# Performance work log

Hardware: AMD Instinct MI355X
Metric: run time of the kernel (lower is better)

The kernel has to match this reference:

```python
import jax, jax.numpy as jnp
import numpy as np

B, T, M, P = 256, 256, 256, 256  # batch, timesteps, encoder hidden m, decoder hidden p


def setup_inputs() -> dict:
    key = jax.random.key(0)
    ks = jax.random.split(key, 12)
    def n(k, shape, s=0.05):
        return jax.random.normal(k, shape, dtype=jnp.float32) * s
    return {
        "data": n(ks[0], (B, T - 1, 1), 1.0),          # decoder inputs y_1..y_{T-1}
        "encoder_h": n(ks[1], (B, T, M), 1.0),          # encoder hidden states
        "h0": jnp.zeros((B, P), jnp.float32),
        "s0": jnp.zeros((B, P), jnp.float32),
        # dense: Dense(1) on concat([x, context]) -> input dim 1+M
        "Wd": n(ks[2], (1 + M, 1)), "bd": jnp.zeros((1,), jnp.float32),
        # decoder LSTM (Keras gate order i,f,c,o): kernel (1,4P), recurrent (P,4P)
        "Wk": n(ks[3], (1, 4 * P)), "Wr": n(ks[4], (P, 4 * P)), "bl": jnp.zeros((4 * P,), jnp.float32),
        # temporal attention: W: 2P->M, U: M->M, v: M->1
        "Ww": n(ks[5], (2 * P, M)), "bw": jnp.zeros((M,), jnp.float32),
        "Wu": n(ks[6], (M, M)), "bu": jnp.zeros((M,), jnp.float32),
        "Wv": n(ks[7], (M, 1)), "bv": jnp.zeros((1,), jnp.float32),
        # output head: densevb: P+M -> 1, denseWb: 1 -> P
        "Wvb": n(ks[8], (P + M, 1)), "bvb": jnp.zeros((1,), jnp.float32),
        "Wwb": n(ks[9], (1, P)), "bwb": jnp.zeros((P,), jnp.float32),
    }


def reference(data, encoder_h, h0, s0, Wd, bd, Wk, Wr, bl, Ww, bw,
              Wu, bu, Wv, bv, Wvb, bvb, Wwb, bwb):
    # Hoist U(encoder_h) out of the time loop: it does not depend on t (same math).
    Ue = encoder_h @ Wu + bu                      # (B, T, M)
    xs = jnp.transpose(data, (1, 0, 2))           # (T-1, B, 1) for scan
    ctx0 = jnp.zeros((data.shape[0], Ue.shape[-1]), data.dtype)  # initial context (B, M)

    def step(carry, x_t):
        h, s, ctx = carry                          # (B,P), (B,P), (B,M)
        # y_tilde = Dense(1)(concat([x_t, context]))
        y = jnp.concatenate([x_t, ctx], axis=-1) @ Wd + bd        # (B, 1)
        # single-step Keras LSTM cell, gates i, f, c, o
        z = y @ Wk + h @ Wr + bl                   # (B, 4P)
        i, f, g, o = jnp.split(z, 4, axis=-1)
        s_new = jax.nn.sigmoid(f) * s + jax.nn.sigmoid(i) * jnp.tanh(g)
        h_new = jax.nn.sigmoid(o) * jnp.tanh(s_new)
        # temporal attention: l = v(tanh(W(repeat(concat[h,s])) + U(encoder_h)))
        dsc = jnp.concatenate([h_new, s_new], axis=-1) @ Ww + bw  # (B, M)
        l = jnp.tanh(dsc[:, None, :] + Ue) @ Wv + bv              # (B, T, 1)
        beta = jax.nn.softmax(l, axis=1)                          # softmax over time axis
        # context = beta^T @ encoder_h -> (B, M)
        ctx_new = jnp.sum(beta * encoder_h, axis=1)
        return (h_new, s_new, ctx_new), None

    (h, s, ctx), _ = jax.lax.scan(step, (h0, s0, ctx0), xs)
    cat = jnp.concatenate([h, ctx], axis=-1)[:, None, :]          # (B, 1, P+M)
    # denseWb(densevb(concatenated)): (P+M)->1 then 1->P, as in the source
    return (cat @ Wvb + bvb) @ Wwb + bwb                          # (B, 1, P)
```

## Files before the change

kernel.cpp:

```cpp
#include <hip/hip_runtime.h>
#include <hip/hip_bf16.h>

#define B 256
#define T 256
#define M 256
#define P 256
#define TSTEPS 255
#define NT 1024
#define RG 8

typedef unsigned int uint;
typedef _Float16 hf2 __attribute__((ext_vector_type(2)));

#define KEEP4(v) asm volatile("" : "+v"((v).x), "+v"((v).y), "+v"((v).z), "+v"((v).w))

__device__ __forceinline__ float fast_tanh(float x) {
    float e = exp2f(x * 2.885390082f);
    return 1.f - 2.f * __builtin_amdgcn_rcpf(e + 1.f);
}
__device__ __forceinline__ float fast_sigmoid(float x) {
    float e = exp2f(-x * 1.442695041f);
    return __builtin_amdgcn_rcpf(1.f + e);
}

#if defined(__has_builtin)
#if __has_builtin(__builtin_amdgcn_fdot2)
#define HAVE_FDOT2 1
#endif
#endif

__device__ __forceinline__ float dot2(uint a, uint b, float c) {
#ifdef HAVE_FDOT2
    return __builtin_amdgcn_fdot2(__builtin_bit_cast(hf2, a),
                                  __builtin_bit_cast(hf2, b), c, false);
#else
    hf2 x = __builtin_bit_cast(hf2, a), y = __builtin_bit_cast(hf2, b);
    return c + (float)x.x * (float)y.x + (float)x.y * (float)y.y;
#endif
}

__device__ __forceinline__ uint pk16(float a, float b) {
    return __builtin_bit_cast(uint, __builtin_amdgcn_cvt_pkrtz(a, b));
}

__device__ __forceinline__ uint pkmulsq(uint a, uint b) {
    uint p;
    asm("v_pk_mul_f16 %0, %1, %2\n\t"
        "v_pk_mul_f16 %0, %0, %0" : "=v"(p) : "v"(a), "v"(b));
    return p;
}

__device__ __forceinline__ float rcp1p(float x) {
    return __builtin_amdgcn_rcpf(x + 1.f);
}

__device__ __forceinline__ void fsig(int* f, int lane) {
    __threadfence_block();
    if (lane == 0) atomicAdd(f, 1);
}
__device__ __forceinline__ void fwait(int* f, int tgt) {
    while (*(volatile int*)f < tgt) __builtin_amdgcn_s_sleep(1);
    __threadfence_block();
}

__global__ __launch_bounds__(256) void ue_gemm(
    const float* __restrict__ enc, const float* __restrict__ Wu,
    const float* __restrict__ bu, _Float16* __restrict__ Ue16)
{
    __shared__ float At[32][256];
    const int r0 = blockIdx.x * 32;
    const int tid = threadIdx.x;

    #pragma unroll 4
    for (int i = 0; i < 32; ++i)
        At[i][tid] = enc[(size_t)(r0 + i) * 256 + tid];
    __syncthreads();

    float acc[32];
    #pragma unroll
    for (int r = 0; r < 32; ++r) acc[r] = 0.f;

    for (int k = 0; k < 256; k += 4) {
        float w0 = Wu[(size_t)(k + 0) * 256 + tid];
        float w1 = Wu[(size_t)(k + 1) * 256 + tid];
        float w2 = Wu[(size_t)(k + 2) * 256 + tid];
        float w3 = Wu[(size_t)(k + 3) * 256 + tid];
        #pragma unroll
        for (int r = 0; r < 32; ++r) {
            float4 a4 = *(const float4*)&At[r][k];
            acc[r] += a4.x * w0 + a4.y * w1 + a4.z * w2 + a4.w * w3;
        }
    }
    float bub = bu[tid];
    #pragma unroll 4
    for (int r = 0; r < 32; ++r)
        Ue16[(size_t)(r0 + r) * 256 + tid] =
            (_Float16)exp2f(1.442695041f * (acc[r] + bub));
}

__global__ __launch_bounds__(256) void wr_cvt(
    const float* __restrict__ Wr, uint4* __restrict__ Wsz)
{
    int i = blockIdx.x * 256 + threadIdx.x;
    int kc = i >> 10, c = i & 1023;
    const float* s = Wr + (size_t)kc * 8 * 1024 + c;
    uint4 o;
    o.x = pk16(s[0 * 1024], s[1 * 1024]);
    o.y = pk16(s[2 * 1024], s[3 * 1024]);
    o.z = pk16(s[4 * 1024], s[5 * 1024]);
    o.w = pk16(s[6 * 1024], s[7 * 1024]);
    Wsz[i] = o;
}

__global__ __launch_bounds__(256) void ww_cvt(
    const float* __restrict__ Ww, uint4* __restrict__ Wwsz)
{
    int i = blockIdx.x * 256 + threadIdx.x;
    int kk = i >> 8, m = i & 255;
    const float* s = Ww + (size_t)kk * 8 * 256 + m;
    uint4 o;
    o.x = pk16(s[0 * 256], s[1 * 256]);
    o.y = pk16(s[2 * 256], s[3 * 256]);
    o.z = pk16(s[4 * 256], s[5 * 256]);
    o.w = pk16(s[6 * 256], s[7 * 256]);
    Wwsz[i] = o;
}

__global__ __launch_bounds__(NT, 4) void decoder_scan(
    const float* __restrict__ data,
    const float* __restrict__ h0,  const float* __restrict__ s0,
    const float* __restrict__ Wd,  const float* __restrict__ bd,
    const float* __restrict__ Wk,  const float* __restrict__ bl,
    const float* __restrict__ bw,
    const float* __restrict__ Wv,  const float* __restrict__ bv,
    const float* __restrict__ Wvb, const float* __restrict__ bvb,
    const float* __restrict__ Wwb, const float* __restrict__ bwb,
    const float* __restrict__ enc,
    const _Float16* __restrict__ Ue16g,
    const uint4* __restrict__ Wsz, const uint4* __restrict__ Wwsz,
    float* __restrict__ out)
{
    const int b    = blockIdx.x;
    const int tid  = threadIdx.x;
    const int lane = tid & 63;
    const int wave = tid >> 6;

    __shared__ __align__(16) uint4 ww_lds[2 * 16 * 256];
    __shared__ float h_lds[P], s_lds[P];
    __shared__ __align__(16) uint hs2[128 + 4 + 128];
    __shared__ float z_lds[4 * 257];
    __shared__ __align__(16) uint  edup[2][132];
    __shared__ __align__(16) float wv2dup[2][264];
    __shared__ float el_lds[T];
    __shared__ float g_lds[T];
    __shared__ float ctx_lds[M];
    __shared__ __align__(16) float sred[8], yred[8];
    __shared__ float ya[4];
    __shared__ float data_lds[TSTEPS + 1];
    __shared__ int pf, zf, ef, df;

    uint* h2_lds = hs2;
    uint* s2_lds = hs2 + 132;

    {
        #pragma unroll
        for (int k = 0; k < 8; ++k) {
            int l = tid + k * NT;
            int i = l >> 9, r = l & 511, dmm = r >> 1, dk = r & 1;
            ww_lds[l] = Wwsz[((dk * 32 + i) << 8) + dmm];
        }
    }
    if (tid == 0) { pf = 0; zf = 0; ef = 0; df = 0; }
    if (tid < 256) {
        float hv = h0[b * 256 + tid], sv = s0[b * 256 + tid];
        h_lds[tid] = hv; s_lds[tid] = sv; ctx_lds[tid] = 0.f;
        float w2 = 2.f * Wv[tid];
        wv2dup[0][tid] = w2; wv2dup[1][tid] = w2;
        float hv1 = __shfl_down(hv, 1, 64);
        float sv1 = __shfl_down(sv, 1, 64);
        if (!(tid & 1)) {
            h2_lds[tid >> 1] = pk16(hv, hv1);
            s2_lds[tid >> 1] = pk16(sv, sv1);
        }
    }
    if (tid < 8) { sred[tid] = 1.f; yred[tid] = 0.f; }
    if (tid < TSTEPS) data_lds[tid] = data[b * TSTEPS + tid];

    const float Wd0 = Wd[0], bd0 = bd[0];
    const float* encB = enc + (size_t)b * T * M;

    {
        float w0 = Wd[1 + lane * 4], w1 = Wd[2 + lane * 4];
        float w2 = Wd[3 + lane * 4], w3 = Wd[4 + lane * 4];
        for (int i = 0; i < 16; ++i) {
            int tp = wave * 16 + i;
            float4 e4 = *(const float4*)&encB[(size_t)tp * 256 + lane * 4];
            float p = e4.x * w0 + e4.y * w1 + e4.z * w2 + e4.w * w3;
            #pragma unroll
            for (int mm = 32; mm >= 1; mm >>= 1) p += __shfl_xor(p, mm, 64);
            if (lane == 0) g_lds[tp] = p;
        }
    }
    __syncthreads();

    const uint4* h2u4 = (const uint4*)h2_lds;
    const uint4* s2u4 = (const uint4*)s2_lds;

    {
        const uint4* wc = Wsz + tid;
        float acc = 0.f;
        #pragma unroll 4
        for (int kc = 0; kc < 32; ++kc) {
            uint4 w = wc[kc << 10];
            uint4 h = h2u4[kc];
            acc = dot2(w.x, h.x, acc); acc = dot2(w.y, h.y, acc);
            acc = dot2(w.z, h.z, acc); acc = dot2(w.w, h.w, acc);
        }
        z_lds[(tid >> 8) * 257 + (tid & 255)] = acc;
    }
    __syncthreads();

    if (wave < 8) {
        const int gate = tid & 3, uu0 = tid >> 2, uu1 = uu0 + 128;
        const int cz0 = gate * 257 + uu0, cz1 = gate * 257 + uu1;
        const float wk0 = Wk[gate * 256 + uu0], bl0 = bl[gate * 256 + uu0];
        const float wk1 = Wk[gate * 256 + uu1], bl1 = bl[gate * 256 + uu1];
        const int zr = tid >> 8, zc = tid & 255;
        const uint4* wcA = Wsz + tid;
        const uint4* wcB = Wsz + tid + 512;
        uint4 rA[RG], rB[RG];
        #pragma unroll
        for (int kc = 0; kc < RG; ++kc) {
            rA[kc] = wcA[kc << 10]; rB[kc] = wcB[kc << 10];
            KEEP4(rA[kc]); KEEP4(rB[kc]);
        }

        for (int t = 0; t < TSTEPS; ++t) {
            uint4 pA0 = wcA[(RG + 0) << 10], pB0 = wcB[(RG + 0) << 10];
            uint4 pA1 = wcA[(RG + 1) << 10], pB1 = wcB[(RG + 1) << 10];

            fwait(&zf, 8 * t);
            fwait(&ef, 8 * t);
            {
                float4 sa = *(const float4*)&sred[0], sb = *(const float4*)&sred[4];
                float4 yaa = *(const float4*)&yred[0], yab = *(const float4*)&yred[4];
                float S = sa.x + sa.y + sa.z + sa.w + sb.x + sb.y + sb.z + sb.w;
                float Y = yaa.x + yaa.y + yaa.z + yaa.w + yab.x + yab.y + yab.z + yab.w;
                float ys = Y * __builtin_amdgcn_rcpf(S) + data_lds[t] * Wd0 + bd0;
                float zc0 = z_lds[cz0] + ys * wk0 + bl0;
                float zc1 = z_lds[cz1] + ys * wk1 + bl1;
                float nl0 = (gate == 2) ? fast_tanh(zc0) : fast_sigmoid(zc0);
                float nl1 = (gate == 2) ? fast_tanh(zc1) : fast_sigmoid(zc1);
                float a1 = __shfl_xor(nl0, 1, 64);
                float a2 = __shfl_xor(nl0, 2, 64);
                float a3 = __shfl_xor(nl0, 3, 64);
                float b1 = __shfl_xor(nl1, 1, 64);
                float b2 = __shfl_xor(nl1, 2, 64);
                float b3 = __shfl_xor(nl1, 3, 64);
                float hn0 = 0.f, sv0 = 0.f, hn1 = 0.f, sv1 = 0.f;
                if (gate == 0) {
                    sv0 = a1 * s_lds[uu0] + nl0 * a2;
                    hn0 = a3 * fast_tanh(sv0);
                    sv1 = b1 * s_lds[uu1] + nl1 * b2;
                    hn1 = b3 * fast_tanh(sv1);
                    s_lds[uu0] = sv0; h_lds[uu0] = hn0;
                    s_lds[uu1] = sv1; h_lds[uu1] = hn1;
                }
                float hd0 = __shfl_down(hn0, 4, 64), sd0 = __shfl_down(sv0, 4, 64);
                float hd1 = __shfl_down(hn1, 4, 64), sd1 = __shfl_down(sv1, 4, 64);
                if ((tid & 7) == 0) {
                    h2_lds[uu0 >> 1] = pk16(hn0, hd0); s2_lds[uu0 >> 1] = pk16(sv0, sd0);
                    h2_lds[uu1 >> 1] = pk16(hn1, hd1); s2_lds[uu1 >> 1] = pk16(sv1, sd1);
                }
            }
            fsig(&pf, lane);
            fwait(&pf, 8 * (t + 1));

            float a0 = 0.f, a1 = 0.f;
            #pragma unroll
            for (int kc = 0; kc < RG; ++kc) {
                uint4 h = h2u4[kc];
                a0 = dot2(rA[kc].x, h.x, a0); a0 = dot2(rA[kc].y, h.y, a0);
                a0 = dot2(rA[kc].z, h.z, a0); a0 = dot2(rA[kc].w, h.w, a0);
                a1 = dot2(rB[kc].x, h.x, a1); a1 = dot2(rB[kc].y, h.y, a1);
                a1 = dot2(rB[kc].z, h.z, a1); a1 = dot2(rB[kc].w, h.w, a1);
            }
            {
                uint4 h = h2u4[RG];
                a0 = dot2(pA0.x, h.x, a0); a0 = dot2(pA0.y, h.y, a0);
                a0 = dot2(pA0.z, h.z, a0); a0 = dot2(pA0.w, h.w, a0);
                a1 = dot2(pB0.x, h.x, a1); a1 = dot2(pB0.y, h.y, a1);
                a1 = dot2(pB0.z, h.z, a1); a1 = dot2(pB0.w, h.w, a1);
            }
            {
                uint4 h = h2u4[RG + 1];
                a0 = dot2(pA1.x, h.x, a0); a0 = dot2(pA1.y, h.y, a0);
                a0 = dot2(pA1.z, h.z, a0); a0 = dot2(pA1.w, h.w, a0);
                a1 = dot2(pB1.x, h.x, a1); a1 = dot2(pB1.y, h.y, a1);
                a1 = dot2(pB1.z, h.z, a1); a1 = dot2(pB1.w, h.w, a1);
            }
            #pragma unroll 4
            for (int kc = RG + 2; kc < 32; ++kc) {
                uint4 wA = wcA[kc << 10], wB = wcB[kc << 10];
                uint4 h = h2u4[kc];
                a0 = dot2(wA.x, h.x, a0); a0 = dot2(wA.y, h.y, a0);
                a0 = dot2(wA.z, h.z, a0); a0 = dot2(wA.w, h.w, a0);
                a1 = dot2(wB.x, h.x, a1); a1 = dot2(wB.y, h.y, a1);
                a1 = dot2(wB.z, h.z, a1); a1 = dot2(wB.w, h.w, a1);
            }
            z_lds[zr * 257 + zc] = a0;
            z_lds[(2 + zr) * 257 + zc] = a1;
            fsig(&zf, lane);
        }
    } else {
        const int aw  = wave - 8;
        const int aid = tid - 512;
        const int dm  = aid >> 1;
        const int dkh = aid & 1;
        const float bwm = bw[dm];
        const uint4* wwp  = Wwsz + (dkh << 13) + dm;
        const uint4* wwl  = ww_lds + aid;
        const uint4*  edT = (const uint4*)(&edup[dkh][0]) + (dkh << 4);
        const float4* wvT = (const float4*)(&wv2dup[dkh][0]) + (dkh << 5);
        const uint4* cat4 = dkh ? s2u4 : h2u4;

        uint4 eu[16];
        {
            const uint4* eusrc = (const uint4*)(Ue16g + (size_t)b * T * M) + (aid << 4);
            #pragma unroll
            for (int i = 0; i < 16; ++i) { eu[i] = eusrc[i]; KEEP4(eu[i]); }
        }

        for (int t = 0; t < TSTEPS; ++t) {
            uint4 e0 = wwp[16 << 8], e1 = wwp[17 << 8];
            uint4 e2 = wwp[18 << 8], e3 = wwp[19 << 8];
            fwait(&pf, 8 * (t + 1));
            float a = 0.f;
            #pragma unroll 4
            for (int i = 0; i < 16; ++i) {
                uint4 w = wwl[i << 9];
                uint4 c = cat4[i];
                a = dot2(w.x, c.x, a); a = dot2(w.y, c.y, a);
                a = dot2(w.z, c.z, a); a = dot2(w.w, c.w, a);
            }
            {
                uint4 c = cat4[16];
                a = dot2(e0.x, c.x, a); a = dot2(e0.y, c.y, a);
                a = dot2(e0.z, c.z, a); a = dot2(e0.w, c.w, a);
                c = cat4[17];
                a = dot2(e1.x, c.x, a); a = dot2(e1.y, c.y, a);
                a = dot2(e1.z, c.z, a); a = dot2(e1.w, c.w, a);
                c = cat4[18];
                a = dot2(e2.x, c.x, a); a = dot2(e2.y, c.y, a);
                a = dot2(e2.z, c.z, a); a = dot2(e2.w, c.w, a);
                c = cat4[19];
                a = dot2(e3.x, c.x, a); a = dot2(e3.y, c.y, a);
                a = dot2(e3.z, c.z, a); a = dot2(e3.w, c.w, a);
            }
            #pragma unroll 4
            for (int i = 20; i < 32; ++i) {
                uint4 w = wwp[i << 8];
                uint4 c = cat4[i];
                a = dot2(w.x, c.x, a); a = dot2(w.y, c.y, a);
                a = dot2(w.z, c.z, a); a = dot2(w.w, c.w, a);
            }
            a += __shfl_xor(a, 1, 64);
            float ed = exp2f(1.442695041f * (a + bwm));
            float ed2 = __shfl_xor(ed, 2, 64);
            if ((aid & 3) == 0) {
                uint u = pk16(ed, ed2);
                edup[0][dm >> 1] = u;
                edup[1][dm >> 1] = u;
            }
            fsig(&df, lane);
            fwait(&df, 8 * (t + 1));

            __builtin_amdgcn_s_setprio(1);
            float pl = 0.f;
            #pragma unroll
            for (int jj = 0; jj < 16; ++jj) {
                uint4 u = eu[jj];
                uint4 d = edT[jj];
                float4 wA = wvT[jj * 2], wB = wvT[jj * 2 + 1];
                uint q0 = pkmulsq(u.x, d.x);
                uint q1 = pkmulsq(u.y, d.y);
                uint q2 = pkmulsq(u.z, d.z);
                uint q3 = pkmulsq(u.w, d.w);
                hf2 g0 = __builtin_bit_cast(hf2, q0);
                hf2 g1 = __builtin_bit_cast(hf2, q1);
                hf2 g2 = __builtin_bit_cast(hf2, q2);
                hf2 g3 = __builtin_bit_cast(hf2, q3);
                pl = fmaf(wA.x, rcp1p((float)g0.x), pl);
                pl = fmaf(wA.y, rcp1p((float)g0.y), pl);
                pl = fmaf(wA.z, rcp1p((float)g1.x), pl);
                pl = fmaf(wA.w, rcp1p((float)g1.y), pl);
                pl = fmaf(wB.x, rcp1p((float)g2.x), pl);
                pl = fmaf(wB.y, rcp1p((float)g2.y), pl);
                pl = fmaf(wB.z, rcp1p((float)g3.x), pl);
                pl = fmaf(wB.w, rcp1p((float)g3.y), pl);
            }
            pl += __shfl_xor(pl, 1, 64);
            float ev = exp2f(-1.442695041f * pl);
            if (!dkh) el_lds[dm] = ev;
            float yg = ev * g_lds[dm];
            #pragma unroll
            for (int mm = 2; mm <= 32; mm <<= 1) {
                ev += __shfl_xor(ev, mm, 64);
                yg += __shfl_xor(yg, mm, 64);
            }
            if (lane == 0) { sred[aw] = ev; yred[aw] = yg; }
            __builtin_amdgcn_s_setprio(0);
            fsig(&ef, lane);
        }
    }

    __syncthreads();

    {
        float S;
        {
            float4 sa = *(const float4*)&sred[0], sb = *(const float4*)&sred[4];
            S = sa.x + sa.y + sa.z + sa.w + sb.x + sb.y + sb.z + sb.w;
        }
        float a0 = 0.f, a1 = 0.f, a2 = 0.f, a3 = 0.f;
        for (int i = 0; i < 16; ++i) {
            int tp = wave * 16 + i;
            float w = el_lds[tp];
            float4 e4 = *(const float4*)&encB[(size_t)tp * 256 + lane * 4];
            a0 += w * e4.x; a1 += w * e4.y; a2 += w * e4.z; a3 += w * e4.w;
        }
        atomicAdd(&ctx_lds[lane * 4 + 0], a0);
        atomicAdd(&ctx_lds[lane * 4 + 1], a1);
        atomicAdd(&ctx_lds[lane * 4 + 2], a2);
        atomicAdd(&ctx_lds[lane * 4 + 3], a3);
        __syncthreads();

        float qp = 0.f;
        if (tid < 256) {
            float ctx = ctx_lds[tid] * __builtin_amdgcn_rcpf(S);
            qp = h_lds[tid] * Wvb[tid] + ctx * Wvb[256 + tid];
        }
        if (wave < 4) {
            #pragma unroll
            for (int mm = 32; mm >= 1; mm >>= 1) qp += __shfl_xor(qp, mm, 64);
            if (lane == 0) ya[wave] = qp;
        }
        __syncthreads();
        if (tid < 256) {
            float qv = ya[0] + ya[1] + ya[2] + ya[3] + bvb[0];
            out[b * 256 + tid] = qv * Wwb[tid] + bwb[tid];
        }
    }
}

extern "C" void kernel_launch(void* const* d_in, const int* in_sizes, int n_in,
                              void* d_out, int out_size, void* d_ws, size_t ws_size,
                              hipStream_t stream) {
    const float* data = (const float*)d_in[0];
    const float* enc  = (const float*)d_in[1];
    const float* h0   = (const float*)d_in[2];
    const float* s0   = (const float*)d_in[3];
    const float* Wd   = (const float*)d_in[4];
    const float* bd   = (const float*)d_in[5];
    const float* Wk   = (const float*)d_in[6];
    const float* Wr   = (const float*)d_in[7];
    const float* bl   = (const float*)d_in[8];
    const float* Ww   = (const float*)d_in[9];
    const float* bw   = (const float*)d_in[10];
    const float* Wu   = (const float*)d_in[11];
    const float* bu   = (const float*)d_in[12];
    const float* Wv   = (const float*)d_in[13];
    const float* bv   = (const float*)d_in[14];
    const float* Wvb  = (const float*)d_in[15];
    const float* bvb  = (const float*)d_in[16];
    const float* Wwb  = (const float*)d_in[17];
    const float* bwb  = (const float*)d_in[18];

    _Float16* Ue16 = (_Float16*)d_ws;
    uint4* Wsz  = (uint4*)((char*)d_ws + (32ull << 20));
    uint4* Wwsz = (uint4*)((char*)d_ws + (32ull << 20) + (512ull << 10));
    float* out = (float*)d_out;

    hipLaunchKernelGGL(ue_gemm, dim3((B * T) / 32), dim3(256), 0, stream,
                       enc, Wu, bu, Ue16);
    hipLaunchKernelGGL(wr_cvt, dim3(128), dim3(256), 0, stream, Wr, Wsz);
    hipLaunchKernelGGL(ww_cvt, dim3(64), dim3(256), 0, stream, Ww, Wwsz);
    hipLaunchKernelGGL(decoder_scan, dim3(B), dim3(NT), 0, stream,
                       data, h0, s0, Wd, bd, Wk, bl, bw,
                       Wv, bv, Wvb, bvb, Wwb, bwb,
                       enc, Ue16, Wsz, Wwsz, out);
}
```

Before: 2.395 ms.

## Pin resident weights in AGPRs and software-pipeline streamed recurrent weight loads

Register-resident Wr slices and half of the cached Ue16 values are now held in accumulator registers (AGPRs) rather than VGPRs, and the resident chunk count drops from 8 to 4. The remaining recurrent-weight chunks are streamed in groups of four, with the next group's global loads issued before the current group's dot products, so load latency overlaps compute. The inline-asm packed multiply is replaced by plain half-vector multiplies the compiler can schedule. The cost is more global weight traffic per step and possible AGPR-to-VGPR copies on every use.

```diff
diff --git a/kernel.cpp b/kernel.cpp
--- a/kernel.cpp
+++ b/kernel.cpp
@@ -7,12 +7,13 @@
 #define P 256
 #define TSTEPS 255
 #define NT 1024
-#define RG 8
+#define RG 4
 
 typedef unsigned int uint;
 typedef _Float16 hf2 __attribute__((ext_vector_type(2)));
 
-#define KEEP4(v) asm volatile("" : "+v"((v).x), "+v"((v).y), "+v"((v).z), "+v"((v).w))
+#define KEEP4A(v) asm volatile("" : "+a"((v).x), "+a"((v).y), "+a"((v).z), "+a"((v).w))
+#define KEEP4V(v) asm volatile("" : "+v"((v).x), "+v"((v).y), "+v"((v).z), "+v"((v).w))
 
 __device__ __forceinline__ float fast_tanh(float x) {
     float e = exp2f(x * 2.885390082f);
@@ -41,13 +42,6 @@
 
 __device__ __forceinline__ uint pk16(float a, float b) {
     return __builtin_bit_cast(uint, __builtin_amdgcn_cvt_pkrtz(a, b));
-}
-
-__device__ __forceinline__ uint pkmulsq(uint a, uint b) {
-    uint p;
-    asm("v_pk_mul_f16 %0, %1, %2\n\t"
-        "v_pk_mul_f16 %0, %0, %0" : "=v"(p) : "v"(a), "v"(b));
-    return p;
 }
 
 __device__ __forceinline__ float rcp1p(float x) {
@@ -232,12 +226,15 @@
         #pragma unroll
         for (int kc = 0; kc < RG; ++kc) {
             rA[kc] = wcA[kc << 10]; rB[kc] = wcB[kc << 10];
-            KEEP4(rA[kc]); KEEP4(rB[kc]);
+            KEEP4A(rA[kc]); KEEP4A(rB[kc]);
         }
 
         for (int t = 0; t < TSTEPS; ++t) {
-            uint4 pA0 = wcA[(RG + 0) << 10], pB0 = wcB[(RG + 0) << 10];
-            uint4 pA1 = wcA[(RG + 1) << 10], pB1 = wcB[(RG + 1) << 10];
+            uint4 sA[4], sB[4];
+            #pragma unroll
+            for (int i = 0; i < 4; ++i) {
+                sA[i] = wcA[(RG + i) << 10]; sB[i] = wcB[(RG + i) << 10];
+            }
 
             fwait(&zf, 8 * t);
             fwait(&ef, 8 * t);
@@ -285,28 +282,26 @@
                 a1 = dot2(rB[kc].x, h.x, a1); a1 = dot2(rB[kc].y, h.y, a1);
                 a1 = dot2(rB[kc].z, h.z, a1); a1 = dot2(rB[kc].w, h.w, a1);
             }
-            {
-                uint4 h = h2u4[RG];
-                a0 = dot2(pA0.x, h.x, a0); a0 = dot2(pA0.y, h.y, a0);
-                a0 = dot2(pA0.z, h.z, a0); a0 = dot2(pA0.w, h.w, a0);
-                a1 = dot2(pB0.x, h.x, a1); a1 = dot2(pB0.y, h.y, a1);
-                a1 = dot2(pB0.z, h.z, a1); a1 = dot2(pB0.w, h.w, a1);
-            }
-            {
-                uint4 h = h2u4[RG + 1];
-                a0 = dot2(pA1.x, h.x, a0); a0 = dot2(pA1.y, h.y, a0);
-                a0 = dot2(pA1.z, h.z, a0); a0 = dot2(pA1.w, h.w, a0);
-                a1 = dot2(pB1.x, h.x, a1); a1 = dot2(pB1.y, h.y, a1);
-                a1 = dot2(pB1.z, h.z, a1); a1 = dot2(pB1.w, h.w, a1);
-            }
-            #pragma unroll 4
-            for (int kc = RG + 2; kc < 32; ++kc) {
-                uint4 wA = wcA[kc << 10], wB = wcB[kc << 10];
-                uint4 h = h2u4[kc];
-                a0 = dot2(wA.x, h.x, a0); a0 = dot2(wA.y, h.y, a0);
-                a0 = dot2(wA.z, h.z, a0); a0 = dot2(wA.w, h.w, a0);
-                a1 = dot2(wB.x, h.x, a1); a1 = dot2(wB.y, h.y, a1);
-                a1 = dot2(wB.z, h.z, a1); a1 = dot2(wB.w, h.w, a1);
+            #pragma unroll
+            for (int g = 0; g < 7; ++g) {
+                uint4 nA[4], nB[4];
+                if (g < 6) {
+                    #pragma unroll
+                    for (int i = 0; i < 4; ++i) {
+                        nA[i] = wcA[(RG + 4 * (g + 1) + i) << 10];
+                        nB[i] = wcB[(RG + 4 * (g + 1) + i) << 10];
+                    }
+                }
+                #pragma unroll
+                for (int i = 0; i < 4; ++i) {
+                    uint4 h = h2u4[RG + 4 * g + i];
+                    a0 = dot2(sA[i].x, h.x, a0); a0 = dot2(sA[i].y, h.y, a0);
+                    a0 = dot2(sA[i].z, h.z, a0); a0 = dot2(sA[i].w, h.w, a0);
+                    a1 = dot2(sB[i].x, h.x, a1); a1 = dot2(sB[i].y, h.y, a1);
+                    a1 = dot2(sB[i].z, h.z, a1); a1 = dot2(sB[i].w, h.w, a1);
+                }
+                #pragma unroll
+                for (int i = 0; i < 4; ++i) { sA[i] = nA[i]; sB[i] = nB[i]; }
             }
             z_lds[zr * 257 + zc] = a0;
             z_lds[(2 + zr) * 257 + zc] = a1;
@@ -328,7 +323,9 @@
         {
             const uint4* eusrc = (const uint4*)(Ue16g + (size_t)b * T * M) + (aid << 4);
             #pragma unroll
-            for (int i = 0; i < 16; ++i) { eu[i] = eusrc[i]; KEEP4(eu[i]); }
+            for (int i = 0; i < 8; ++i)  { eu[i] = eusrc[i]; KEEP4A(eu[i]); }
+            #pragma unroll
+            for (int i = 8; i < 16; ++i) { eu[i] = eusrc[i]; KEEP4V(eu[i]); }
         }
 
         for (int t = 0; t < TSTEPS; ++t) {
@@ -382,14 +379,11 @@
                 uint4 u = eu[jj];
                 uint4 d = edT[jj];
                 float4 wA = wvT[jj * 2], wB = wvT[jj * 2 + 1];
-                uint q0 = pkmulsq(u.x, d.x);
-                uint q1 = pkmulsq(u.y, d.y);
-                uint q2 = pkmulsq(u.z, d.z);
-                uint q3 = pkmulsq(u.w, d.w);
-                hf2 g0 = __builtin_bit_cast(hf2, q0);
-                hf2 g1 = __builtin_bit_cast(hf2, q1);
-                hf2 g2 = __builtin_bit_cast(hf2, q2);
-                hf2 g3 = __builtin_bit_cast(hf2, q3);
+                hf2 g0 = __builtin_bit_cast(hf2, u.x) * __builtin_bit_cast(hf2, d.x);
+                hf2 g1 = __builtin_bit_cast(hf2, u.y) * __builtin_bit_cast(hf2, d.y);
+                hf2 g2 = __builtin_bit_cast(hf2, u.z) * __builtin_bit_cast(hf2, d.z);
+                hf2 g3 = __builtin_bit_cast(hf2, u.w) * __builtin_bit_cast(hf2, d.w);
+                g0 = g0 * g0; g1 = g1 * g1; g2 = g2 * g2; g3 = g3 * g3;
                 pl = fmaf(wA.x, rcp1p((float)g0.x), pl);
                 pl = fmaf(wA.y, rcp1p((float)g0.y), pl);
                 pl = fmaf(wA.z, rcp1p((float)g1.x), pl);
```

Result: slower. 6.081 ms (+153.9%).
